# Kernel optimization log

Measured on AMD Instinct MI355X. Metric: run time of the kernel, lower is better.

Reference implementation:

```python
import jax, jax.numpy as jnp
import numpy as np
from jax import lax

B, S, E, H = 4, 1024, 512, 8
D = E // H


def setup_inputs() -> dict:
    key = jax.random.key(0)
    k1, k2, k3 = jax.random.split(key, 3)
    source = jax.random.normal(k1, (B, S, E), dtype=jnp.float32)
    target = jax.random.normal(k2, (B, S, E), dtype=jnp.float32)
    # orthogonal-initialized positional encoder [1, H, 1, D]; random rows are a fine stand-in
    enc = jax.random.normal(k3, (1, H, 1, D), dtype=jnp.float32)
    enc = enc / jnp.linalg.norm(enc, axis=-1, keepdims=True)
    return {
        "source": source,
        "target": target,
        "encoder": enc,
        "alpha": jnp.float32(1.0),
        "beta": jnp.float32(1.0),
        "gamma": jnp.float32(2.0),
    }


def _split_heads(x):
    b, s, e = x.shape
    return x.reshape(b, s, H, e // H).transpose(0, 2, 1, 3)  # [B,H,S,D]


def reference(source, target, encoder, alpha, beta, gamma):
    q = _split_heads(source)  # [B,H,S,D]
    k = _split_heads(target)  # [B,H,S,D]
    pe = encoder[0, :, 0, :]  # [H,D]

    # --- grammar (time) attention: sequential tanh recurrence over t ---
    def step(cc, k_t):
        # cc, k_t: [B,H,D]
        cc = jnp.tanh(cc * pe)
        out = jnp.einsum('bhsd,bhd->bhs', q, cc)  # [B,H,S]
        return k_t * cc, out  # decay_rate = 0.0

    cc0 = k[:, :, 0, :]                      # initial cumulative context
    k_ts = jnp.moveaxis(k, 2, 0)             # [S,B,H,D]
    _, outs = lax.scan(step, cc0, k_ts)      # outs: [S,B,H,S]
    grammar = jnp.moveaxis(outs, 0, 3) / jnp.sqrt(jnp.float32(D))  # [B,H,S,S]
    grammar = jax.nn.softmax(grammar, axis=-1)

    # --- semantic attention ---
    semantic = jnp.einsum('bhsd,bhtd->bhst', q, k) / 100.0  # [B,H,S,S]

    w = jax.nn.softmax((alpha * semantic + beta * grammar) / gamma, axis=-1)

    # merge_heads: [B,H,S,S] -> [B,S,H*S]
    wm = w.transpose(0, 2, 1, 3).reshape(B, S, H * S)
    # output: wm^T @ target -> [B, H*S, E]
    return jnp.matmul(wm.transpose(0, 2, 1), target)
```

## Files before the change

kernel.cpp:

```cpp
#include <hip/hip_runtime.h>
#include <hip/hip_bf16.h>
#include <stdint.h>

#define S_LEN 1024
#define E_DIM 512
#define H_NUM 8
#define D_DIM 64
#define B_NUM 4
#define BH_NUM 32

using s16x8 = __attribute__((ext_vector_type(8))) short;
using f32x4 = __attribute__((ext_vector_type(4))) float;
using us4   = __attribute__((ext_vector_type(4))) unsigned short;

static __device__ __forceinline__ unsigned short f2bf(float f) {
  __hip_bfloat16 h = __float2bfloat16(f);
  return __builtin_bit_cast(unsigned short, h);
}
static __device__ __forceinline__ float bf2f(unsigned short u) {
  return __bfloat162float(__builtin_bit_cast(__hip_bfloat16, u));
}

#define NB_RECUR 8
#define NB_PACK  8192
#define NB_TR    512

__global__ __launch_bounds__(256) void k_prep(const float* __restrict__ src,
                                              const float* __restrict__ tgt,
                                              const float* __restrict__ enc,
                                              __hip_bfloat16* __restrict__ qb,
                                              __hip_bfloat16* __restrict__ kb,
                                              __hip_bfloat16* __restrict__ cb,
                                              __hip_bfloat16* __restrict__ tT) {
  __shared__ float tile[64][65];
  const int bid = blockIdx.x;
  const int tid = threadIdx.x;

  if (bid < NB_RECUR) {
    int g = bid * 256 + tid;
    int d = g & 63;
    int bh = g >> 6;
    int h = bh & 7;
    int b = bh >> 3;
    float pe = enc[h * D_DIM + d];
    float pe2 = 2.0f * pe;
    const float* tp = tgt + (size_t)b * S_LEN * E_DIM + h * D_DIM + d;
    __hip_bfloat16* cp = cb + (size_t)bh * S_LEN * D_DIM + d;

    constexpr int CH = 32;
    float bufA[CH], bufB[CH];
#pragma unroll
    for (int i = 0; i < CH; ++i) bufA[i] = tp[(size_t)i * E_DIM];
    float cc = bufA[0];

#pragma unroll 1
    for (int ch = 0; ch < S_LEN / CH; ch += 2) {
      if (ch + 1 < S_LEN / CH) {
#pragma unroll
        for (int i = 0; i < CH; ++i)
          bufB[i] = tp[(size_t)((ch + 1) * CH + i) * E_DIM];
      }
#pragma unroll
      for (int i = 0; i < CH; ++i) {
        float m = cc * pe2;
        float e = __expf(-fabsf(m));
        float th = __builtin_copysignf((1.0f - e) * __builtin_amdgcn_rcpf(1.0f + e), m);
        cp[(size_t)(ch * CH + i) * D_DIM] = __float2bfloat16(th);
        cc = bufA[i] * th;
      }
      if (ch + 2 < S_LEN / CH) {
#pragma unroll
        for (int i = 0; i < CH; ++i)
          bufA[i] = tp[(size_t)((ch + 2) * CH + i) * E_DIM];
      }
#pragma unroll
      for (int i = 0; i < CH; ++i) {
        float m = cc * pe2;
        float e = __expf(-fabsf(m));
        float th = __builtin_copysignf((1.0f - e) * __builtin_amdgcn_rcpf(1.0f + e), m);
        cp[(size_t)((ch + 1) * CH + i) * D_DIM] = __float2bfloat16(th);
        cc = bufB[i] * th;
      }
    }
  } else if (bid < NB_RECUR + NB_PACK) {
    size_t i = (size_t)(bid - NB_RECUR) * 256 + tid;
    int e = (int)(i & 511);
    size_t bs = i >> 9;
    int s = (int)(bs & 1023);
    int b = (int)(bs >> 10);
    int h = e >> 6, d = e & 63;
    size_t o = (((size_t)(b * H_NUM + h) * S_LEN) + s) * D_DIM + d;
    qb[o] = __float2bfloat16(src[i]);
    kb[o] = __float2bfloat16(tgt[i]);
  } else {
    int lb = bid - (NB_RECUR + NB_PACK);
    int sx = lb & 15, ey = (lb >> 4) & 7, b = lb >> 7;
    int e0 = ey * 64, s0 = sx * 64;
    int tx = tid & 63, ty = tid >> 6;
    const float* p = tgt + ((size_t)b * S_LEN + s0) * E_DIM + e0;
#pragma unroll
    for (int r = ty; r < 64; r += 4) tile[r][tx] = p[(size_t)r * E_DIM + tx];
    __syncthreads();
    __hip_bfloat16* q = tT + ((size_t)b * E_DIM + e0) * S_LEN + s0;
#pragma unroll
    for (int r = ty; r < 64; r += 4) q[(size_t)r * S_LEN + tx] = __float2bfloat16(tile[tx][r]);
  }
}

__global__ __launch_bounds__(256) void k_weights(const __hip_bfloat16* __restrict__ qb,
                                                 const __hip_bfloat16* __restrict__ kb,
                                                 const __hip_bfloat16* __restrict__ cb,
                                                 __hip_bfloat16* __restrict__ wt,
                                                 const float* __restrict__ pal,
                                                 const float* __restrict__ pbe,
                                                 const float* __restrict__ pga) {
  __shared__ __hip_bfloat16 zl[S_LEN * 16];
  __shared__ float red0[4][16];
  __shared__ float red1[4][16];

  const int tid = threadIdx.x;
  const int wave = tid >> 6, lane = tid & 63;
  const int quad = lane >> 4, col = lane & 15;
  const int bh = blockIdx.y;
  const int s0 = blockIdx.x * 16;

  const float alpha = pal[0], beta = pbe[0];
  const float inv_gamma = 1.0f / pga[0];
  const float sa = alpha * 0.01f * inv_gamma;
  const float sb = beta * inv_gamma;

  const __hip_bfloat16* qrow = qb + ((size_t)bh * S_LEN + s0 + col) * D_DIM;
  s16x8 a0 = *reinterpret_cast<const s16x8*>(qrow + quad * 8);
  s16x8 a1 = *reinterpret_cast<const s16x8*>(qrow + 32 + quad * 8);

  const int t_base = wave * 256;

  const __hip_bfloat16* cbh = cb + (size_t)bh * S_LEN * D_DIM;
  float lg[4] = {0.f, 0.f, 0.f, 0.f};
#pragma unroll 4
  for (int it = 0; it < 16; ++it) {
    int t0 = t_base + it * 16;
    const __hip_bfloat16* crow = cbh + (size_t)(t0 + col) * D_DIM;
    s16x8 b0 = *reinterpret_cast<const s16x8*>(crow + quad * 8);
    s16x8 b1 = *reinterpret_cast<const s16x8*>(crow + 32 + quad * 8);
    f32x4 dacc = {0.f, 0.f, 0.f, 0.f};
    dacc = __builtin_amdgcn_mfma_f32_16x16x32_bf16(a0, b0, dacc, 0, 0, 0);
    dacc = __builtin_amdgcn_mfma_f32_16x16x32_bf16(a1, b1, dacc, 0, 0, 0);
    us4 pk;
#pragma unroll
    for (int i = 0; i < 4; ++i) {
      float g = __expf(dacc[i] * 0.125f);
      unsigned short u = f2bf(g);
      pk[i] = u;
      lg[i] += bf2f(u);
    }
    *reinterpret_cast<us4*>(&zl[(size_t)(t0 + col) * 16 + quad * 4]) = pk;
  }
#pragma unroll
  for (int m = 1; m < 16; m <<= 1) {
#pragma unroll
    for (int i = 0; i < 4; ++i) lg[i] += __shfl_xor(lg[i], m);
  }
  if (col == 0) {
#pragma unroll
    for (int i = 0; i < 4; ++i) red0[wave][quad * 4 + i] = lg[i];
  }
  __syncthreads();
  float ilg[4];
#pragma unroll
  for (int i = 0; i < 4; ++i) {
    int r = quad * 4 + i;
    ilg[i] = 1.0f / (red0[0][r] + red0[1][r] + red0[2][r] + red0[3][r]);
  }

  const __hip_bfloat16* kbh = kb + (size_t)bh * S_LEN * D_DIM;
  float lw[4] = {0.f, 0.f, 0.f, 0.f};
#pragma unroll 4
  for (int it = 0; it < 16; ++it) {
    int t0 = t_base + it * 16;
    const __hip_bfloat16* krow = kbh + (size_t)(t0 + col) * D_DIM;
    s16x8 b0 = *reinterpret_cast<const s16x8*>(krow + quad * 8);
    s16x8 b1 = *reinterpret_cast<const s16x8*>(krow + 32 + quad * 8);
    f32x4 dacc = {0.f, 0.f, 0.f, 0.f};
    dacc = __builtin_amdgcn_mfma_f32_16x16x32_bf16(a0, b0, dacc, 0, 0, 0);
    dacc = __builtin_amdgcn_mfma_f32_16x16x32_bf16(a1, b1, dacc, 0, 0, 0);
    size_t zidx = (size_t)(t0 + col) * 16 + quad * 4;
    us4 pk = *reinterpret_cast<const us4*>(&zl[zidx]);
    us4 onew;
#pragma unroll
    for (int i = 0; i < 4; ++i) {
      float g = bf2f(pk[i]) * ilg[i];
      float z = sa * dacc[i] + sb * g;
      float wv = __expf(z);
      unsigned short u = f2bf(wv);
      onew[i] = u;
      lw[i] += bf2f(u);
    }
    *reinterpret_cast<us4*>(&zl[zidx]) = onew;
  }
#pragma unroll
  for (int m = 1; m < 16; m <<= 1) {
#pragma unroll
    for (int i = 0; i < 4; ++i) lw[i] += __shfl_xor(lw[i], m);
  }
  if (col == 0) {
#pragma unroll
    for (int i = 0; i < 4; ++i) red1[wave][quad * 4 + i] = lw[i];
  }
  __syncthreads();
  float ilw[4];
#pragma unroll
  for (int i = 0; i < 4; ++i) {
    int r = quad * 4 + i;
    ilw[i] = 1.0f / (red1[0][r] + red1[1][r] + red1[2][r] + red1[3][r]);
  }

#pragma unroll 4
  for (int it = 0; it < 16; ++it) {
    int t0 = t_base + it * 16;
    us4 pk = *reinterpret_cast<const us4*>(&zl[(size_t)(t0 + col) * 16 + quad * 4]);
    us4 o;
#pragma unroll
    for (int i = 0; i < 4; ++i) o[i] = f2bf(bf2f(pk[i]) * ilw[i]);
    *reinterpret_cast<us4*>(wt + ((size_t)bh * S_LEN + (t0 + col)) * S_LEN + s0 + quad * 4) = o;
  }
}

typedef const __attribute__((address_space(1))) uint32_t gas_uint;
typedef __attribute__((address_space(3))) uint32_t las_uint;

__global__ __launch_bounds__(256) void k_outgemm(const __hip_bfloat16* __restrict__ wt,
                                                 const __hip_bfloat16* __restrict__ tT,
                                                 float* __restrict__ out) {
  __shared__ __hip_bfloat16 As[128 * 64];
  __shared__ __hip_bfloat16 Bs[128 * 64];
  const int tid = threadIdx.x;
  const int wave = tid >> 6, lane = tid & 63;
  const int quad = lane >> 4, col = lane & 15;
  const int bh = blockIdx.z;
  const int b = bh >> 3;
  const int m0 = blockIdx.y * 128;
  const int n0 = blockIdx.x * 128;
  const __hip_bfloat16* Ag = wt + (size_t)bh * S_LEN * S_LEN;
  const __hip_bfloat16* Bg = tT + (size_t)b * E_DIM * S_LEN;
  const int mw = (wave >> 1) * 64, nw = (wave & 1) * 64;
  const int lrow = lane >> 3;
  const int lcol = (lane & 7) * 8;

  f32x4 acc[4][4];
#pragma unroll
  for (int i = 0; i < 4; ++i)
#pragma unroll
    for (int j = 0; j < 4; ++j) acc[i][j] = (f32x4){0.f, 0.f, 0.f, 0.f};

  for (int kt = 0; kt < 16; ++kt) {
    const int k0 = kt * 64;
    __syncthreads();
#pragma unroll
    for (int j = 0; j < 4; ++j) {
      int row = j * 32 + wave * 8 + lrow;
      const __hip_bfloat16* gp = Ag + (size_t)(m0 + row) * S_LEN + k0 + lcol;
      __builtin_amdgcn_global_load_lds((gas_uint*)gp,
                                       (las_uint*)(As + (j * 32 + wave * 8) * 64),
                                       16, 0, 0);
    }
#pragma unroll
    for (int j = 0; j < 4; ++j) {
      int row = j * 32 + wave * 8 + lrow;
      const __hip_bfloat16* gp = Bg + (size_t)(n0 + row) * S_LEN + k0 + lcol;
      __builtin_amdgcn_global_load_lds((gas_uint*)gp,
                                       (las_uint*)(Bs + (j * 32 + wave * 8) * 64),
                                       16, 0, 0);
    }
    __syncthreads();
#pragma unroll
    for (int ks = 0; ks < 2; ++ks) {
      s16x8 af[4], bf[4];
#pragma unroll
      for (int i = 0; i < 4; ++i)
        af[i] = *reinterpret_cast<const s16x8*>(As + (mw + i * 16 + col) * 64 + ks * 32 + quad * 8);
#pragma unroll
      for (int i = 0; i < 4; ++i)
        bf[i] = *reinterpret_cast<const s16x8*>(Bs + (nw + i * 16 + col) * 64 + ks * 32 + quad * 8);
#pragma unroll
      for (int mi = 0; mi < 4; ++mi)
#pragma unroll
        for (int ni = 0; ni < 4; ++ni)
          acc[mi][ni] = __builtin_amdgcn_mfma_f32_16x16x32_bf16(af[mi], bf[ni], acc[mi][ni], 0, 0, 0);
    }
  }

#pragma unroll
  for (int mi = 0; mi < 4; ++mi)
#pragma unroll
    for (int ni = 0; ni < 4; ++ni)
#pragma unroll
      for (int i = 0; i < 4; ++i) {
        int m = m0 + mw + mi * 16 + quad * 4 + i;
        int n = n0 + nw + ni * 16 + col;
        out[((size_t)bh * S_LEN + m) * E_DIM + n] = acc[mi][ni][i];
      }
}

extern "C" void kernel_launch(void* const* d_in, const int* in_sizes, int n_in,
                              void* d_out, int out_size, void* d_ws, size_t ws_size,
                              hipStream_t stream) {
  (void)in_sizes; (void)n_in; (void)out_size; (void)ws_size;
  const float* src = (const float*)d_in[0];
  const float* tgt = (const float*)d_in[1];
  const float* enc = (const float*)d_in[2];
  const float* pal = (const float*)d_in[3];
  const float* pbe = (const float*)d_in[4];
  const float* pga = (const float*)d_in[5];
  float* out = (float*)d_out;

  char* ws = (char*)d_ws;
  __hip_bfloat16* qb = (__hip_bfloat16*)(ws);
  __hip_bfloat16* kb = (__hip_bfloat16*)(ws + ((size_t)4 << 20));
  __hip_bfloat16* cb = (__hip_bfloat16*)(ws + ((size_t)8 << 20));
  __hip_bfloat16* tT = (__hip_bfloat16*)(ws + ((size_t)12 << 20));
  __hip_bfloat16* wt = (__hip_bfloat16*)(ws + ((size_t)16 << 20));

  k_prep<<<NB_RECUR + NB_PACK + NB_TR, 256, 0, stream>>>(src, tgt, enc, qb, kb, cb, tT);
  k_weights<<<dim3(S_LEN / 16, BH_NUM), 256, 0, stream>>>(qb, kb, cb, wt, pal, pbe, pga);
  k_outgemm<<<dim3(E_DIM / 128, S_LEN / 128, BH_NUM), 256, 0, stream>>>(wt, tT, out);
}
```

Baseline: 247.8 us.

## Vectorize packing, keep softmax scores in registers, remap GEMM blocks per XCD

```diff
diff --git a/kernel.cpp b/kernel.cpp
--- a/kernel.cpp
+++ b/kernel.cpp
@@ -17,12 +17,9 @@
   __hip_bfloat16 h = __float2bfloat16(f);
   return __builtin_bit_cast(unsigned short, h);
 }
-static __device__ __forceinline__ float bf2f(unsigned short u) {
-  return __bfloat162float(__builtin_bit_cast(__hip_bfloat16, u));
-}
 
 #define NB_RECUR 8
-#define NB_PACK  8192
+#define NB_PACK  2048
 #define NB_TR    512
 
 __global__ __launch_bounds__(256) void k_prep(const float* __restrict__ src,
@@ -83,15 +80,19 @@
       }
     }
   } else if (bid < NB_RECUR + NB_PACK) {
-    size_t i = (size_t)(bid - NB_RECUR) * 256 + tid;
-    int e = (int)(i & 511);
-    size_t bs = i >> 9;
+    size_t i4 = ((size_t)(bid - NB_RECUR) * 256 + tid) * 4;
+    float4 s4 = *reinterpret_cast<const float4*>(src + i4);
+    float4 t4 = *reinterpret_cast<const float4*>(tgt + i4);
+    int e = (int)(i4 & 511);
+    size_t bs = i4 >> 9;
     int s = (int)(bs & 1023);
     int b = (int)(bs >> 10);
     int h = e >> 6, d = e & 63;
     size_t o = (((size_t)(b * H_NUM + h) * S_LEN) + s) * D_DIM + d;
-    qb[o] = __float2bfloat16(src[i]);
-    kb[o] = __float2bfloat16(tgt[i]);
+    us4 qv = {f2bf(s4.x), f2bf(s4.y), f2bf(s4.z), f2bf(s4.w)};
+    us4 kv = {f2bf(t4.x), f2bf(t4.y), f2bf(t4.z), f2bf(t4.w)};
+    *reinterpret_cast<us4*>(qb + o) = qv;
+    *reinterpret_cast<us4*>(kb + o) = kv;
   } else {
     int lb = bid - (NB_RECUR + NB_PACK);
     int sx = lb & 15, ey = (lb >> 4) & 7, b = lb >> 7;
@@ -114,7 +115,6 @@
                                                  const float* __restrict__ pal,
                                                  const float* __restrict__ pbe,
                                                  const float* __restrict__ pga) {
-  __shared__ __hip_bfloat16 zl[S_LEN * 16];
   __shared__ float red0[4][16];
   __shared__ float red1[4][16];
 
@@ -134,27 +134,24 @@
   s16x8 a1 = *reinterpret_cast<const s16x8*>(qrow + 32 + quad * 8);
 
   const int t_base = wave * 256;
-
-  const __hip_bfloat16* cbh = cb + (size_t)bh * S_LEN * D_DIM;
+  float st[16][4];
+
+  const __hip_bfloat16* cbh = cb + ((size_t)bh * S_LEN + t_base + col) * D_DIM;
   float lg[4] = {0.f, 0.f, 0.f, 0.f};
-#pragma unroll 4
+#pragma unroll
   for (int it = 0; it < 16; ++it) {
-    int t0 = t_base + it * 16;
-    const __hip_bfloat16* crow = cbh + (size_t)(t0 + col) * D_DIM;
+    const __hip_bfloat16* crow = cbh + (size_t)it * 16 * D_DIM;
     s16x8 b0 = *reinterpret_cast<const s16x8*>(crow + quad * 8);
     s16x8 b1 = *reinterpret_cast<const s16x8*>(crow + 32 + quad * 8);
     f32x4 dacc = {0.f, 0.f, 0.f, 0.f};
     dacc = __builtin_amdgcn_mfma_f32_16x16x32_bf16(a0, b0, dacc, 0, 0, 0);
     dacc = __builtin_amdgcn_mfma_f32_16x16x32_bf16(a1, b1, dacc, 0, 0, 0);
-    us4 pk;
 #pragma unroll
     for (int i = 0; i < 4; ++i) {
       float g = __expf(dacc[i] * 0.125f);
-      unsigned short u = f2bf(g);
-      pk[i] = u;
-      lg[i] += bf2f(u);
-    }
-    *reinterpret_cast<us4*>(&zl[(size_t)(t0 + col) * 16 + quad * 4]) = pk;
+      st[it][i] = g;
+      lg[i] += g;
+    }
   }
 #pragma unroll
   for (int m = 1; m < 16; m <<= 1) {
@@ -173,30 +170,23 @@
     ilg[i] = 1.0f / (red0[0][r] + red0[1][r] + red0[2][r] + red0[3][r]);
   }
 
-  const __hip_bfloat16* kbh = kb + (size_t)bh * S_LEN * D_DIM;
+  const __hip_bfloat16* kbh = kb + ((size_t)bh * S_LEN + t_base + col) * D_DIM;
   float lw[4] = {0.f, 0.f, 0.f, 0.f};
-#pragma unroll 4
+#pragma unroll
   for (int it = 0; it < 16; ++it) {
-    int t0 = t_base + it * 16;
-    const __hip_bfloat16* krow = kbh + (size_t)(t0 + col) * D_DIM;
+    const __hip_bfloat16* krow = kbh + (size_t)it * 16 * D_DIM;
     s16x8 b0 = *reinterpret_cast<const s16x8*>(krow + quad * 8);
     s16x8 b1 = *reinterpret_cast<const s16x8*>(krow + 32 + quad * 8);
     f32x4 dacc = {0.f, 0.f, 0.f, 0.f};
     dacc = __builtin_amdgcn_mfma_f32_16x16x32_bf16(a0, b0, dacc, 0, 0, 0);
     dacc = __builtin_amdgcn_mfma_f32_16x16x32_bf16(a1, b1, dacc, 0, 0, 0);
-    size_t zidx = (size_t)(t0 + col) * 16 + quad * 4;
-    us4 pk = *reinterpret_cast<const us4*>(&zl[zidx]);
-    us4 onew;
 #pragma unroll
     for (int i = 0; i < 4; ++i) {
-      float g = bf2f(pk[i]) * ilg[i];
-      float z = sa * dacc[i] + sb * g;
+      float z = sa * dacc[i] + sb * (st[it][i] * ilg[i]);
       float wv = __expf(z);
-      unsigned short u = f2bf(wv);
-      onew[i] = u;
-      lw[i] += bf2f(u);
-    }
-    *reinterpret_cast<us4*>(&zl[zidx]) = onew;
+      st[it][i] = wv;
+      lw[i] += wv;
+    }
   }
 #pragma unroll
   for (int m = 1; m < 16; m <<= 1) {
@@ -215,14 +205,13 @@
     ilw[i] = 1.0f / (red1[0][r] + red1[1][r] + red1[2][r] + red1[3][r]);
   }
 
-#pragma unroll 4
+  __hip_bfloat16* wrow = wt + ((size_t)bh * S_LEN + t_base + col) * S_LEN + s0 + quad * 4;
+#pragma unroll
   for (int it = 0; it < 16; ++it) {
-    int t0 = t_base + it * 16;
-    us4 pk = *reinterpret_cast<const us4*>(&zl[(size_t)(t0 + col) * 16 + quad * 4]);
     us4 o;
 #pragma unroll
-    for (int i = 0; i < 4; ++i) o[i] = f2bf(bf2f(pk[i]) * ilw[i]);
-    *reinterpret_cast<us4*>(wt + ((size_t)bh * S_LEN + (t0 + col)) * S_LEN + s0 + quad * 4) = o;
+    for (int i = 0; i < 4; ++i) o[i] = f2bf(st[it][i] * ilw[i]);
+    *reinterpret_cast<us4*>(wrow + (size_t)it * 16 * S_LEN) = o;
   }
 }
 
@@ -237,10 +226,18 @@
   const int tid = threadIdx.x;
   const int wave = tid >> 6, lane = tid & 63;
   const int quad = lane >> 4, col = lane & 15;
-  const int bh = blockIdx.z;
+
+  const int g = blockIdx.x;
+  const int xcd = g & 7;
+  const int local = g >> 3;
+  const int strip = xcd * 32 + (local >> 2);
+  const int ntile = local & 3;
+  const int bh = strip >> 3;
+  const int mt = strip & 7;
   const int b = bh >> 3;
-  const int m0 = blockIdx.y * 128;
-  const int n0 = blockIdx.x * 128;
+  const int m0 = mt * 128;
+  const int n0 = ntile * 128;
+
   const __hip_bfloat16* Ag = wt + (size_t)bh * S_LEN * S_LEN;
   const __hip_bfloat16* Bg = tT + (size_t)b * E_DIM * S_LEN;
   const int mw = (wave >> 1) * 64, nw = (wave & 1) * 64;
@@ -323,5 +320,5 @@
 
   k_prep<<<NB_RECUR + NB_PACK + NB_TR, 256, 0, stream>>>(src, tgt, enc, qb, kb, cb, tT);
   k_weights<<<dim3(S_LEN / 16, BH_NUM), 256, 0, stream>>>(qb, kb, cb, wt, pal, pbe, pga);
-  k_outgemm<<<dim3(E_DIM / 128, S_LEN / 128, BH_NUM), 256, 0, stream>>>(wt, tT, out);
-}
+  k_outgemm<<<dim3((E_DIM / 128) * (S_LEN / 128) * BH_NUM), 256, 0, stream>>>(wt, tT, out);
+}
```

After: 248.6 us. No clear change (+0.3%).
